# Optimization experiments

Hardware: AMD Instinct MI355X
Metric: run time of the kernel (lower is better)

## Reference

```python
import jax, jax.numpy as jnp
import numpy as np

NEG = -9e15
ALPHA = 0.2  # leaky relu slope

def setup_inputs() -> dict:
    key = jax.random.key(0)
    k1, k2, k3, k4 = jax.random.split(key, 4)
    N, Fin, Fout = 8192, 512, 256
    h = jax.random.normal(k1, (N, Fin), dtype=jnp.float32)
    adj = jax.random.randint(k2, (N, N), 0, 2, dtype=jnp.int32)
    # xavier_uniform with gain=1.414
    gain = 1.414
    limW = gain * np.sqrt(6.0 / (Fin + Fout))
    W = jax.random.uniform(k3, (Fin, Fout), dtype=jnp.float32, minval=-limW, maxval=limW)
    lima = gain * np.sqrt(6.0 / (2 * Fout + 1))
    a = jax.random.uniform(k4, (2 * Fout, 1), dtype=jnp.float32, minval=-lima, maxval=lima)
    return {"h": h, "adj": adj, "W": W, "a": a}

def reference(h, adj, W, a):
    Fout = W.shape[1]
    Wh = h @ W                                   # [N, Fout]
    # decompose a = [a1; a2]: e_ij = leaky(a1.Wh_i + a2.Wh_j)
    f1 = Wh @ a[:Fout]                           # [N, 1]
    f2 = Wh @ a[Fout:]                           # [N, 1]
    e = jax.nn.leaky_relu(f1 + f2.T, negative_slope=ALPHA)  # [N, N]
    e = jnp.where(adj > 0, e, jnp.float32(NEG))
    attention = jax.nn.softmax(e, axis=1)
    # dropout is identity at inference (training=False)
    h_prime = attention @ Wh                     # [N, Fout]
    return jax.nn.elu(h_prime)
```

## Files before the change

### kernel.cpp

```cpp
#include <hip/hip_runtime.h>
#include <cstdint>
#include <cstddef>

#define ALPHA 0.2f

typedef __attribute__((ext_vector_type(8)))  short short8;
typedef __attribute__((ext_vector_type(16))) float f32x16;

static __device__ __forceinline__ unsigned short f2bf(float x) {
  union { float f; unsigned u; } c; c.f = x;
  unsigned u = c.u;
  unsigned r = (u + 0x7FFFu + ((u >> 16) & 1u)) >> 16;
  return (unsigned short)r;
}
static __device__ __forceinline__ float bf2f(unsigned short b) {
  union { unsigned u; float f; } c; c.u = ((unsigned)b) << 16;
  return c.f;
}

__global__ __launch_bounds__(256, 2) void gemm1(const float* __restrict__ h,
                                                const float* __restrict__ W,
                                                float* __restrict__ Wh) {
  __shared__ float As[32][132];
  __shared__ float Bs[32][64];
  const int t = threadIdx.x;
  const int bid = blockIdx.x;
  const int nb = bid & 3, mb = bid >> 2;
  const int m0 = mb * 128, n0 = nb * 64;
  const int ty = t >> 4, tx = t & 15;
  float acc[8][4];
#pragma unroll
  for (int i = 0; i < 8; i++)
#pragma unroll
    for (int j = 0; j < 4; j++) acc[i][j] = 0.f;

  for (int k0 = 0; k0 < 512; k0 += 32) {
#pragma unroll
    for (int c = 0; c < 4; c++) {
      int m = c * 32 + (t >> 3);
      int kq = (t & 7) * 4;
      float4 v = *(const float4*)&h[(size_t)(m0 + m) * 512 + k0 + kq];
      As[kq + 0][m] = v.x; As[kq + 1][m] = v.y;
      As[kq + 2][m] = v.z; As[kq + 3][m] = v.w;
    }
#pragma unroll
    for (int c = 0; c < 2; c++) {
      int k = c * 16 + (t >> 4);
      int n = (t & 15) * 4;
      *(float4*)&Bs[k][n] = *(const float4*)&W[(size_t)(k0 + k) * 256 + n0 + n];
    }
    __syncthreads();
#pragma unroll
    for (int k = 0; k < 32; k++) {
      float4 a0 = *(float4*)&As[k][ty * 8];
      float4 a1 = *(float4*)&As[k][ty * 8 + 4];
      float4 b  = *(float4*)&Bs[k][tx * 4];
      float av[8] = {a0.x, a0.y, a0.z, a0.w, a1.x, a1.y, a1.z, a1.w};
      float bv[4] = {b.x, b.y, b.z, b.w};
#pragma unroll
      for (int i = 0; i < 8; i++)
#pragma unroll
        for (int j = 0; j < 4; j++) acc[i][j] = fmaf(av[i], bv[j], acc[i][j]);
    }
    __syncthreads();
  }
#pragma unroll
  for (int i = 0; i < 8; i++) {
    float4 v = {acc[i][0], acc[i][1], acc[i][2], acc[i][3]};
    *(float4*)&Wh[(size_t)(m0 + ty * 8 + i) * 256 + n0 + tx * 4] = v;
  }
}

__global__ __launch_bounds__(256) void rowstats(const float* __restrict__ Wh,
                                                const float* __restrict__ a,
                                                float* __restrict__ f1,
                                                float* __restrict__ f2,
                                                unsigned* __restrict__ uvpack,
                                                unsigned short* __restrict__ WhT) {
  const int t = threadIdx.x;
  const int w = t >> 6, lane = t & 63;
  const int i = blockIdx.x * 4 + w;
  float4 wv = *(const float4*)&Wh[(size_t)i * 256 + lane * 4];
  float4 a1 = *(const float4*)&a[lane * 4];
  float4 a2 = *(const float4*)&a[256 + lane * 4];
  float s1 = wv.x * a1.x + wv.y * a1.y + wv.z * a1.z + wv.w * a1.w;
  float s2 = wv.x * a2.x + wv.y * a2.y + wv.z * a2.z + wv.w * a2.w;
#pragma unroll
  for (int off = 32; off; off >>= 1) { s1 += __shfl_xor(s1, off); s2 += __shfl_xor(s2, off); }
  const float wvv[4] = {wv.x, wv.y, wv.z, wv.w};
#pragma unroll
  for (int c = 0; c < 4; c++)
    WhT[(size_t)(lane * 4 + c) * 8192 + i] = f2bf(wvv[c]);
  if (lane == 0) {
    f1[i] = s1; f2[i] = s2;
    float u = __expf(s2), v = __expf(ALPHA * s2);
    uvpack[i] = (unsigned)f2bf(u) | ((unsigned)f2bf(v) << 16);
  }
}

__global__ __launch_bounds__(256) void f2max_k(const float* __restrict__ f2,
                                               float* __restrict__ f2maxp) {
  __shared__ float red[256];
  const int t = threadIdx.x;
  float m = -1e30f;
  for (int c = 0; c < 32; c++) m = fmaxf(m, f2[c * 256 + t]);
  red[t] = m;
  __syncthreads();
  for (int s = 128; s; s >>= 1) {
    if (t < s) red[t] = fmaxf(red[t], red[t + s]);
    __syncthreads();
  }
  if (t == 0) f2maxp[0] = red[0];
}

__global__ __launch_bounds__(256, 2) void attn_main(const int* __restrict__ adj,
                                                    const float* __restrict__ f1,
                                                    const unsigned* __restrict__ uvpack,
                                                    const unsigned short* __restrict__ WhT,
                                                    const float* __restrict__ f2maxp,
                                                    float* __restrict__ accP,
                                                    float* __restrict__ lP) {
  __shared__ unsigned uvs[4096];
  __shared__ __align__(16) unsigned short Pt[32][40];
  __shared__ float lred[32][8];
  const int t = threadIdx.x;
  const int bid = blockIdx.x;
  const int jh = bid & 1;
  const int rb = bid >> 1;
  const int r0 = rb * 32;
  const int jbase = jh * 4096;

#pragma unroll
  for (int c = 0; c < 4; c++) {
    int idx = c * 1024 + t * 4;
    *(uint4*)&uvs[idx] = *(const uint4*)&uvpack[jbase + idx];
  }

  const int r = t >> 3, q = t & 7;
  const float F2max = f2maxp[0];
  const float f1v = f1[r0 + r];
  const float x = f1v + F2max;
  const float M = x > 0.f ? x : ALPHA * x;
  const float Ai = __expf(f1v - M);
  const float Bi = __expf(ALPHA * f1v - M);
  const float Ui = __expf(-f1v);

  const int lane = t & 63, wave = t >> 6;
  const int am = lane & 31, asel = lane >> 5;
  f32x16 acc0 = {}; f32x16 acc1 = {};
  float lpriv = 0.f;

  const int* adjp = adj + (size_t)(r0 + r) * 8192 + jbase + q * 4;
  const unsigned short* bp0 = WhT + (size_t)(wave * 64 + am) * 8192 + jbase + asel * 8;
  const unsigned short* bp1 = bp0 + (size_t)32 * 8192;

  __syncthreads();

  int4 av = *(const int4*)adjp; adjp += 32;
  for (int s = 0; s < 128; s++) {
    int4 avn;
    if (s < 127) { avn = *(const int4*)adjp; }
    adjp += 32;
    uint4 uvq = *(const uint4*)&uvs[s * 32 + q * 4];
    const unsigned uv[4] = {uvq.x, uvq.y, uvq.z, uvq.w};
    const int ad[4] = {av.x, av.y, av.z, av.w};
    float wgt[4];
#pragma unroll
    for (int jj = 0; jj < 4; jj++) {
      float u = bf2f((unsigned short)(uv[jj] & 0xFFFFu));
      float v = bf2f((unsigned short)(uv[jj] >> 16));
      float wv = (u > Ui) ? Ai * u : Bi * v;
      wv = (ad[jj] > 0) ? wv : 0.f;
      wgt[jj] = wv;
    }
    lpriv += (wgt[0] + wgt[1]) + (wgt[2] + wgt[3]);
    unsigned p0 = (unsigned)f2bf(wgt[0]) | ((unsigned)f2bf(wgt[1]) << 16);
    unsigned p1 = (unsigned)f2bf(wgt[2]) | ((unsigned)f2bf(wgt[3]) << 16);
    uint2 pw; pw.x = p0; pw.y = p1;
    *(uint2*)&Pt[r][q * 4] = pw;
    __syncthreads();
#pragma unroll
    for (int hh = 0; hh < 2; hh++) {
      short8 afrag = *(const short8*)&Pt[am][hh * 16 + asel * 8];
      short8 bf0 = *(const short8*)(bp0 + (size_t)s * 32 + hh * 16);
      short8 bf1 = *(const short8*)(bp1 + (size_t)s * 32 + hh * 16);
      acc0 = __builtin_amdgcn_mfma_f32_32x32x16_bf16(afrag, bf0, acc0, 0, 0, 0);
      acc1 = __builtin_amdgcn_mfma_f32_32x32x16_bf16(afrag, bf1, acc1, 0, 0, 0);
    }
    __syncthreads();
    av = avn;
  }

  const size_t base = (size_t)jh * (8192 * 256);
#pragma unroll
  for (int reg = 0; reg < 16; reg++) {
    int rowl = (reg & 3) + 8 * (reg >> 2) + 4 * asel;
    int col = wave * 64 + am;
    accP[base + (size_t)(r0 + rowl) * 256 + col] = acc0[reg];
    accP[base + (size_t)(r0 + rowl) * 256 + col + 32] = acc1[reg];
  }
  lred[r][q] = lpriv;
  __syncthreads();
  if (q == 0) {
    float ssum = 0.f;
#pragma unroll
    for (int k = 0; k < 8; k++) ssum += lred[r][k];
    lP[jh * 8192 + r0 + r] = ssum;
  }
}

__global__ __launch_bounds__(256) void combine(const float* __restrict__ accP,
                                               const float* __restrict__ lP,
                                               float* __restrict__ out) {
  const int idx = (blockIdx.x * 256 + threadIdx.x) * 4;
  const int row = idx >> 8;
  float4 a0 = *(const float4*)&accP[idx];
  float4 a1 = *(const float4*)&accP[(size_t)8192 * 256 + idx];
  float l = lP[row] + lP[8192 + row];
  float inv = 1.0f / fmaxf(l, 1e-30f);
  float vv[4] = {(a0.x + a1.x) * inv, (a0.y + a1.y) * inv,
                 (a0.z + a1.z) * inv, (a0.w + a1.w) * inv};
  float4 o;
  o.x = vv[0] > 0.f ? vv[0] : __expf(vv[0]) - 1.f;
  o.y = vv[1] > 0.f ? vv[1] : __expf(vv[1]) - 1.f;
  o.z = vv[2] > 0.f ? vv[2] : __expf(vv[2]) - 1.f;
  o.w = vv[3] > 0.f ? vv[3] : __expf(vv[3]) - 1.f;
  *(float4*)&out[idx] = o;
}

extern "C" void kernel_launch(void* const* d_in, const int* in_sizes, int n_in,
                              void* d_out, int out_size, void* d_ws, size_t ws_size,
                              hipStream_t stream) {
  const float* h  = (const float*)d_in[0];
  const int* adj  = (const int*)d_in[1];
  const float* W  = (const float*)d_in[2];
  const float* a  = (const float*)d_in[3];
  float* out = (float*)d_out;
  char* ws = (char*)d_ws;

  float* Wh            = (float*)ws;
  float* accP          = (float*)ws;
  unsigned short* WhT  = (unsigned short*)(ws + (size_t)(16u << 20));
  float* f1            = (float*)(ws + (size_t)(20u << 20));
  float* f2            = (float*)(ws + (size_t)(20u << 20) + (32u << 10));
  unsigned* uvpack     = (unsigned*)(ws + (size_t)(20u << 20) + (64u << 10));
  float* f2maxp        = (float*)(ws + (size_t)(20u << 20) + (96u << 10));
  float* lP            = (float*)(ws + (size_t)(20u << 20) + (97u << 10));

  gemm1<<<256, 256, 0, stream>>>(h, W, Wh);
  rowstats<<<2048, 256, 0, stream>>>(Wh, a, f1, f2, uvpack, WhT);
  f2max_k<<<1, 256, 0, stream>>>(f2, f2maxp);
  attn_main<<<512, 256, 0, stream>>>(adj, f1, uvpack, WhT, f2maxp, accP, lP);
  combine<<<2048, 256, 0, stream>>>(accP, lP, out);
}
```

Before: 558.3 us.

## Restructure attention kernel into per-wave full-width tiles with split-j atomic reduction

Each wave now owns 32 rows across all 256 output columns and computes its attention weights directly in the MFMA A-operand layout. This removes the LDS staging of weights and uv values, and the two barriers per step. The j dimension is split eight ways instead of two, and partial results are combined with float atomics into accP and lP, which a new zeroing kernel clears first. The combine kernel reads a single accumulator. In exchange the kernel holds 128 accumulator registers per lane, issues many global atomics at the end, and adds one extra launch.

```diff
diff --git a/kernel.cpp b/kernel.cpp
--- a/kernel.cpp
+++ b/kernel.cpp
@@ -113,6 +113,17 @@
   if (t == 0) f2maxp[0] = red[0];
 }
 
+__global__ __launch_bounds__(256) void zerok(float* __restrict__ accP,
+                                             float* __restrict__ lP) {
+  const int b = blockIdx.x, t = threadIdx.x;
+  float4 z = {0.f, 0.f, 0.f, 0.f};
+  if (b < 2048) {
+    *(float4*)&accP[((size_t)b * 256 + t) * 4] = z;
+  } else {
+    *(float4*)&lP[((size_t)(b - 2048) * 256 + t) * 4] = z;
+  }
+}
+
 __global__ __launch_bounds__(256, 2) void attn_main(const int* __restrict__ adj,
                                                     const float* __restrict__ f1,
                                                     const unsigned* __restrict__ uvpack,
@@ -120,92 +131,83 @@
                                                     const float* __restrict__ f2maxp,
                                                     float* __restrict__ accP,
                                                     float* __restrict__ lP) {
-  __shared__ unsigned uvs[4096];
-  __shared__ __align__(16) unsigned short Pt[32][40];
-  __shared__ float lred[32][8];
-  const int t = threadIdx.x;
+  const int t = threadIdx.x;
+  const int wave = t >> 6, lane = t & 63;
   const int bid = blockIdx.x;
-  const int jh = bid & 1;
-  const int rb = bid >> 1;
-  const int r0 = rb * 32;
-  const int jbase = jh * 4096;
-
-#pragma unroll
-  for (int c = 0; c < 4; c++) {
-    int idx = c * 1024 + t * 4;
-    *(uint4*)&uvs[idx] = *(const uint4*)&uvpack[jbase + idx];
-  }
-
-  const int r = t >> 3, q = t & 7;
+  const int js = bid & 7;
+  const int rg = bid >> 3;
+  const int r0 = rg * 128 + wave * 32;
+  const int jbase = js * 1024;
+  const int am = lane & 31, asel = lane >> 5;
+  const int row = r0 + am;
+  const int joff = asel * 8;
+
   const float F2max = f2maxp[0];
-  const float f1v = f1[r0 + r];
+  const float f1v = f1[row];
   const float x = f1v + F2max;
   const float M = x > 0.f ? x : ALPHA * x;
   const float Ai = __expf(f1v - M);
   const float Bi = __expf(ALPHA * f1v - M);
   const float Ui = __expf(-f1v);
 
-  const int lane = t & 63, wave = t >> 6;
-  const int am = lane & 31, asel = lane >> 5;
-  f32x16 acc0 = {}; f32x16 acc1 = {};
+  f32x16 acc[8] = {};
+
+  const int* adjp = adj + (size_t)row * 8192 + jbase + joff;
+  const unsigned* uvp = uvpack + jbase + joff;
+  const unsigned short* wtp = WhT + (size_t)am * 8192 + jbase + joff;
+
   float lpriv = 0.f;
-
-  const int* adjp = adj + (size_t)(r0 + r) * 8192 + jbase + q * 4;
-  const unsigned short* bp0 = WhT + (size_t)(wave * 64 + am) * 8192 + jbase + asel * 8;
-  const unsigned short* bp1 = bp0 + (size_t)32 * 8192;
-
-  __syncthreads();
-
-  int4 av = *(const int4*)adjp; adjp += 32;
-  for (int s = 0; s < 128; s++) {
-    int4 avn;
-    if (s < 127) { avn = *(const int4*)adjp; }
-    adjp += 32;
-    uint4 uvq = *(const uint4*)&uvs[s * 32 + q * 4];
-    const unsigned uv[4] = {uvq.x, uvq.y, uvq.z, uvq.w};
-    const int ad[4] = {av.x, av.y, av.z, av.w};
-    float wgt[4];
-#pragma unroll
-    for (int jj = 0; jj < 4; jj++) {
-      float u = bf2f((unsigned short)(uv[jj] & 0xFFFFu));
-      float v = bf2f((unsigned short)(uv[jj] >> 16));
+  int4 adv0 = *(const int4*)adjp;
+  int4 adv1 = *(const int4*)(adjp + 4);
+  uint4 uvv0 = *(const uint4*)uvp;
+  uint4 uvv1 = *(const uint4*)(uvp + 4);
+
+#pragma unroll 1
+  for (int s = 0; s < 64; s++) {
+    const int4 a0 = adv0, a1 = adv1;
+    const uint4 u0 = uvv0, u1 = uvv1;
+    if (s < 63) {
+      adv0 = *(const int4*)(adjp + (s + 1) * 16);
+      adv1 = *(const int4*)(adjp + (s + 1) * 16 + 4);
+      uvv0 = *(const uint4*)(uvp + (s + 1) * 16);
+      uvv1 = *(const uint4*)(uvp + (s + 1) * 16 + 4);
+    }
+    short8 bf[8];
+#pragma unroll
+    for (int ct = 0; ct < 8; ct++)
+      bf[ct] = *(const short8*)(wtp + (size_t)ct * (32 * 8192) + s * 16);
+
+    const int ad[8] = {a0.x, a0.y, a0.z, a0.w, a1.x, a1.y, a1.z, a1.w};
+    const unsigned uu[8] = {u0.x, u0.y, u0.z, u0.w, u1.x, u1.y, u1.z, u1.w};
+    float w[8];
+#pragma unroll
+    for (int jj = 0; jj < 8; jj++) {
+      float u = bf2f((unsigned short)(uu[jj] & 0xFFFFu));
+      float v = bf2f((unsigned short)(uu[jj] >> 16));
       float wv = (u > Ui) ? Ai * u : Bi * v;
       wv = (ad[jj] > 0) ? wv : 0.f;
-      wgt[jj] = wv;
-    }
-    lpriv += (wgt[0] + wgt[1]) + (wgt[2] + wgt[3]);
-    unsigned p0 = (unsigned)f2bf(wgt[0]) | ((unsigned)f2bf(wgt[1]) << 16);
-    unsigned p1 = (unsigned)f2bf(wgt[2]) | ((unsigned)f2bf(wgt[3]) << 16);
-    uint2 pw; pw.x = p0; pw.y = p1;
-    *(uint2*)&Pt[r][q * 4] = pw;
-    __syncthreads();
-#pragma unroll
-    for (int hh = 0; hh < 2; hh++) {
-      short8 afrag = *(const short8*)&Pt[am][hh * 16 + asel * 8];
-      short8 bf0 = *(const short8*)(bp0 + (size_t)s * 32 + hh * 16);
-      short8 bf1 = *(const short8*)(bp1 + (size_t)s * 32 + hh * 16);
-      acc0 = __builtin_amdgcn_mfma_f32_32x32x16_bf16(afrag, bf0, acc0, 0, 0, 0);
-      acc1 = __builtin_amdgcn_mfma_f32_32x32x16_bf16(afrag, bf1, acc1, 0, 0, 0);
-    }
-    __syncthreads();
-    av = avn;
-  }
-
-  const size_t base = (size_t)jh * (8192 * 256);
-#pragma unroll
-  for (int reg = 0; reg < 16; reg++) {
-    int rowl = (reg & 3) + 8 * (reg >> 2) + 4 * asel;
-    int col = wave * 64 + am;
-    accP[base + (size_t)(r0 + rowl) * 256 + col] = acc0[reg];
-    accP[base + (size_t)(r0 + rowl) * 256 + col + 32] = acc1[reg];
-  }
-  lred[r][q] = lpriv;
-  __syncthreads();
-  if (q == 0) {
-    float ssum = 0.f;
-#pragma unroll
-    for (int k = 0; k < 8; k++) ssum += lred[r][k];
-    lP[jh * 8192 + r0 + r] = ssum;
+      w[jj] = wv;
+    }
+    lpriv += ((w[0] + w[1]) + (w[2] + w[3])) + ((w[4] + w[5]) + (w[6] + w[7]));
+    short8 af;
+#pragma unroll
+    for (int jj = 0; jj < 8; jj++) af[jj] = (short)f2bf(w[jj]);
+
+#pragma unroll
+    for (int ct = 0; ct < 8; ct++)
+      acc[ct] = __builtin_amdgcn_mfma_f32_32x32x16_bf16(af, bf[ct], acc[ct], 0, 0, 0);
+  }
+
+  lpriv += __shfl_xor(lpriv, 32);
+  if (asel == 0) atomicAdd(&lP[row], lpriv);
+
+#pragma unroll
+  for (int ct = 0; ct < 8; ct++) {
+#pragma unroll
+    for (int reg = 0; reg < 16; reg++) {
+      const int rowl = (reg & 3) + 8 * (reg >> 2) + 4 * asel;
+      atomicAdd(&accP[(size_t)(r0 + rowl) * 256 + ct * 32 + am], acc[ct][reg]);
+    }
   }
 }
 
@@ -215,11 +217,9 @@
   const int idx = (blockIdx.x * 256 + threadIdx.x) * 4;
   const int row = idx >> 8;
   float4 a0 = *(const float4*)&accP[idx];
-  float4 a1 = *(const float4*)&accP[(size_t)8192 * 256 + idx];
-  float l = lP[row] + lP[8192 + row];
+  float l = lP[row];
   float inv = 1.0f / fmaxf(l, 1e-30f);
-  float vv[4] = {(a0.x + a1.x) * inv, (a0.y + a1.y) * inv,
-                 (a0.z + a1.z) * inv, (a0.w + a1.w) * inv};
+  float vv[4] = {a0.x * inv, a0.y * inv, a0.z * inv, a0.w * inv};
   float4 o;
   o.x = vv[0] > 0.f ? vv[0] : __expf(vv[0]) - 1.f;
   o.y = vv[1] > 0.f ? vv[1] : __expf(vv[1]) - 1.f;
@@ -250,6 +250,7 @@
   gemm1<<<256, 256, 0, stream>>>(h, W, Wh);
   rowstats<<<2048, 256, 0, stream>>>(Wh, a, f1, f2, uvpack, WhT);
   f2max_k<<<1, 256, 0, stream>>>(f2, f2maxp);
+  zerok<<<2056, 256, 0, stream>>>(accP, lP);
   attn_main<<<512, 256, 0, stream>>>(adj, f1, uvpack, WhT, f2maxp, accP, lP);
   combine<<<2048, 256, 0, stream>>>(accP, lP, out);
 }
```

Measured after the change: 610.3 us. 9.3% more time.
